# Kernel tuning notes

Hardware: AMD Instinct MI355X
Metric: run time of the kernel (lower is better)

## Reference

```python
import jax, jax.numpy as jnp
import numpy as np

B, S, D, P, W = 16, 100, 8192, 100, 3  # batch, seq, feat dim, proj width, window size


def setup_inputs() -> dict:
    key = jax.random.key(0)
    ks = jax.random.split(key, 6)
    return {
        "x": jax.random.normal(ks[0], (B, S, D), dtype=jnp.float32),
        "wq": jax.random.normal(ks[1], (D, P), dtype=jnp.float32) * (1.0 / np.sqrt(D)),
        "wk": jax.random.normal(ks[2], (D, P), dtype=jnp.float32) * (1.0 / np.sqrt(D)),
        "wv": jax.random.normal(ks[3], (D, P), dtype=jnp.float32) * (1.0 / np.sqrt(D)),
        "forwardpad": jax.random.normal(ks[4], (B, 1, D), dtype=jnp.float32),
        "backwardpad": jax.random.normal(ks[5], (B, 1, D), dtype=jnp.float32),
    }


def reference(x, wq, wk, wv, forwardpad, backwardpad):
    # pad: (B, S+2, D)
    padded = jnp.concatenate([forwardpad, x, backwardpad], axis=1)
    # gather all 100 overlapping size-3 windows at once: (B, S, W, D)
    idx = jnp.arange(S)[:, None] + jnp.arange(W)[None, :]  # (S, W)
    windows = padded[:, idx, :]
    # shared projections across all windows (original recomputed per window)
    q = jnp.einsum("bswd,dp->bswp", windows, wq)
    k = jnp.einsum("bswd,dp->bswp", windows, wk)
    v = jnp.einsum("bswd,dp->bswp", windows, wv)
    # per-window 3x3 attention
    scores = jnp.einsum("bswp,bsup->bswu", q, k)  # (B, S, W, W)
    attn = jax.nn.softmax(scores, axis=-1)
    out = jnp.einsum("bswu,bsup->bswp", attn, v)  # (B, S, W, P)
    # original concatenates windows along seq then takes [:, 1::3, :] -> center token of each window
    return out[:, :, 1, :]  # (B, S, P)
```

## Files before the change

kernel.cpp:

```cpp
#include <hip/hip_runtime.h>
#include <hip/hip_bf16.h>
#include <hip/hip_fp16.h>

constexpr int Dk   = 8192;
constexpr int Bb   = 16;
constexpr int Ss   = 100;
constexpr int Pp   = 100;
constexpr int MROW = 1632;
constexpr int NT   = 20;
constexpr int NCC  = 320;
constexpr int NQ   = 304;
constexpr int KG   = 1024;
constexpr int KC   = 16;
constexpr int CH   = 5;
constexpr int MBL  = 52;

constexpr size_t B_SEG   = (size_t)NT * KG * 128;
constexpr size_t PSTRIDE = (size_t)1664 * NCC;

typedef short s8v __attribute__((ext_vector_type(8)));
typedef short s4v __attribute__((ext_vector_type(4)));
typedef float f4v __attribute__((ext_vector_type(4)));

__device__ inline unsigned short f2bf_rne(float f) {
    unsigned u = __float_as_uint(f);
    u += 0x7fffu + ((u >> 16) & 1u);
    return (unsigned short)(u >> 16);
}

__global__ __launch_bounds__(256) void pack_b(
    const float* __restrict__ wq, const float* __restrict__ wk,
    const float* __restrict__ wv,
    short* __restrict__ b_hi, short* __restrict__ b_lo) {
    const int id = blockIdx.x * 256 + threadIdx.x;
    const int n  = id % NCC;
    const int kg = id / NCC;
    if (kg >= KG) return;

    const float* w = nullptr; int p = 0;
    if (n < 100)      { w = wq; p = n; }
    else if (n < 200) { w = wk; p = n - 100; }
    else if (n < 300) { w = wv; p = n - 200; }

    s8v hi, lo;
    #pragma unroll
    for (int j = 0; j < 8; ++j) {
        const float v = w ? w[(size_t)(kg * 8 + j) * Pp + p] : 0.0f;
        const unsigned u = __float_as_uint(v);
        hi[j] = (short)(unsigned short)(u >> 16);
        const float hf = __uint_as_float(u & 0xffff0000u);
        lo[j] = (short)f2bf_rne(v - hf);
    }
    const size_t doff = ((size_t)(n >> 4) * KG + kg) * 128 + (size_t)(n & 15) * 8;
    *(s8v*)(b_hi + doff) = hi;
    *(s8v*)(b_lo + doff) = lo;
}

__global__ __launch_bounds__(256, 2) void qkv_gemm(
    const float* __restrict__ x, const float* __restrict__ fpad,
    const float* __restrict__ bpad,
    const short* __restrict__ b_hi, const short* __restrict__ b_lo,
    unsigned short* __restrict__ part) {
    __shared__ __align__(16) short ahis[2][1024];
    __shared__ __align__(16) short alos[2][1024];

    const int id   = blockIdx.x;
    const int xcd  = id & 7;
    const int slot = id >> 3;
    const int half = (slot >= 52) ? 1 : 0;
    const int kc   = xcd * 2 + half;
    const int mb   = slot - half * 52;

    const int tid  = threadIdx.x;
    const int w    = tid >> 6;
    const int l    = tid & 63;
    const int m    = l & 15;
    const int quad = l >> 4;

    const int sr  = tid >> 3;
    const int skq = tid & 7;
    const float* sp;
    {
        const int r = mb * 32 + sr;
        if (r >= MROW) sp = fpad;
        else {
            const int b = r / 102, rr = r - b * 102;
            if (rr == 0)        sp = fpad + (size_t)b * Dk;
            else if (rr == 101) sp = bpad + (size_t)b * Dk;
            else                sp = x + ((size_t)b * Ss + (rr - 1)) * Dk;
        }
        sp += kc * 512 + skq * 4;
    }
    const int woff = ((sr >> 4) * 4 + (skq >> 1)) * 128 + (sr & 15) * 8 + (skq & 1) * 4;

    float4 av[4];
    #pragma unroll
    for (int p = 0; p < 4; ++p) av[p] = *(const float4*)(sp + p * 32);

    s8v bh[2][5], bl[2][5];
    {
        const int kg0 = kc * 64 + quad;
        #pragma unroll
        for (int j = 0; j < 5; ++j) {
            const size_t bo = ((size_t)(w * 5 + j) * KG + kg0) * 128 + (size_t)m * 8;
            bh[0][j] = *(const s8v*)(b_hi + bo);
            bl[0][j] = *(const s8v*)(b_lo + bo);
        }
    }

    f4v acc[2][5];
    #pragma unroll
    for (int i = 0; i < 2; ++i)
        #pragma unroll
        for (int j = 0; j < 5; ++j) {
            f4v z = {0.f, 0.f, 0.f, 0.f};
            acc[i][j] = z;
        }

    #pragma unroll
    for (int s = 0; s < 16; ++s) {
        const int cur = s & 1, nxt = cur ^ 1;

        const float4 va = av[s & 3];

        if (s < 15) {
            const int kgn = kc * 64 + (s + 1) * 4 + quad;
            #pragma unroll
            for (int j = 0; j < 5; ++j) {
                const size_t bo = ((size_t)(w * 5 + j) * KG + kgn) * 128 + (size_t)m * 8;
                bh[nxt][j] = *(const s8v*)(b_hi + bo);
                bl[nxt][j] = *(const s8v*)(b_lo + bo);
            }
        }
        if (s < 12) av[s & 3] = *(const float4*)(sp + (s + 4) * 32);

        __builtin_amdgcn_sched_barrier(0);

        const float vv[4] = {va.x, va.y, va.z, va.w};
        s4v h4, l4;
        #pragma unroll
        for (int jj = 0; jj < 4; ++jj) {
            const unsigned u = __float_as_uint(vv[jj]);
            h4[jj] = (short)(unsigned short)(u >> 16);
            l4[jj] = (short)f2bf_rne(vv[jj] - __uint_as_float(u & 0xffff0000u));
        }

        *(s4v*)&ahis[cur][woff] = h4;
        *(s4v*)&alos[cur][woff] = l4;

        asm volatile("s_waitcnt lgkmcnt(0)\n\ts_barrier" ::: "memory");

        const s8v ah0 = *(const s8v*)&ahis[cur][(quad * 16 + m) * 8];
        const s8v ah1 = *(const s8v*)&ahis[cur][((4 + quad) * 16 + m) * 8];
        const s8v al0 = *(const s8v*)&alos[cur][(quad * 16 + m) * 8];
        const s8v al1 = *(const s8v*)&alos[cur][((4 + quad) * 16 + m) * 8];

        #pragma unroll
        for (int j = 0; j < 5; ++j) {
            const s8v bhv = bh[cur][j], blv = bl[cur][j];
            acc[0][j] = __builtin_amdgcn_mfma_f32_16x16x32_bf16(ah0, bhv, acc[0][j], 0, 0, 0);
            acc[1][j] = __builtin_amdgcn_mfma_f32_16x16x32_bf16(ah1, bhv, acc[1][j], 0, 0, 0);
            acc[0][j] = __builtin_amdgcn_mfma_f32_16x16x32_bf16(al0, bhv, acc[0][j], 0, 0, 0);
            acc[1][j] = __builtin_amdgcn_mfma_f32_16x16x32_bf16(al1, bhv, acc[1][j], 0, 0, 0);
            acc[0][j] = __builtin_amdgcn_mfma_f32_16x16x32_bf16(ah0, blv, acc[0][j], 0, 0, 0);
            acc[1][j] = __builtin_amdgcn_mfma_f32_16x16x32_bf16(ah1, blv, acc[1][j], 0, 0, 0);
        }
    }

    unsigned short* __restrict__ pout = part + (size_t)kc * PSTRIDE;
    #pragma unroll
    for (int i = 0; i < 2; ++i) {
        #pragma unroll
        for (int j = 0; j < 5; ++j) {
            const int col  = (w * 5 + j) * 16 + m;
            const int row0 = mb * 32 + i * 16 + quad * 4;
            #pragma unroll
            for (int r = 0; r < 4; ++r)
                pout[(size_t)(row0 + r) * NCC + col] =
                    __half_as_ushort(__float2half(acc[i][j][r]));
        }
    }
}

__global__ __launch_bounds__(256) void reduce_k(
    const unsigned short* __restrict__ part, float* __restrict__ qkv) {
    const int t = blockIdx.x * 256 + threadIdx.x;
    const int row = t / 40;
    const int col0 = (t - row * 40) * 8;
    const size_t base = (size_t)row * NCC + col0;

    float sum[8] = {0.f, 0.f, 0.f, 0.f, 0.f, 0.f, 0.f, 0.f};
    #pragma unroll
    for (int k = 0; k < KC; ++k) {
        const s8v u = *(const s8v*)(part + (size_t)k * PSTRIDE + base);
        #pragma unroll
        for (int ii = 0; ii < 8; ++ii)
            sum[ii] += __half2float(__ushort_as_half((unsigned short)u[ii]));
    }
    if (col0 < NQ) {
        f4v a = {sum[0], sum[1], sum[2], sum[3]};
        f4v b = {sum[4], sum[5], sum[6], sum[7]};
        *(f4v*)(qkv + (size_t)row * NQ + col0)     = a;
        *(f4v*)(qkv + (size_t)row * NQ + col0 + 4) = b;
    }
}

__global__ __launch_bounds__(256) void attn3(
    const float* __restrict__ qkv, float* __restrict__ out) {
    const int blk = blockIdx.x;
    const int b  = blk / (Ss / CH);
    const int c  = blk % (Ss / CH);
    const int s0 = c * CH;
    const int tid = threadIdx.x;

    __shared__ float red[CH + 2][304];
    __shared__ float sc[CH][3];

    for (int idx = tid; idx < (CH + 2) * 300; idx += 256) {
        const int row = idx / 300, col = idx % 300;
        red[row][col] = qkv[(size_t)(b * 102 + s0 + row) * NQ + col];
    }
    __syncthreads();

    if (tid < CH * 3 * 16) {
        const int d = tid >> 4, g = tid & 15;
        const int ss = d / 3, u = d % 3;
        float ps = 0.0f;
        #pragma unroll
        for (int t = 0; t < 7; ++t) {
            const int p = g + t * 16;
            if (p < Pp) ps += red[ss + 1][p] * red[ss + u][100 + p];
        }
        #pragma unroll
        for (int off = 8; off > 0; off >>= 1) ps += __shfl_down(ps, off, 16);
        if (g == 0) sc[ss][u] = ps;
    }
    __syncthreads();

    for (int idx = tid; idx < CH * Pp; idx += 256) {
        const int ss = idx / Pp, p = idx % Pp;
        const float a0 = sc[ss][0], a1 = sc[ss][1], a2 = sc[ss][2];
        const float mx = fmaxf(a0, fmaxf(a1, a2));
        const float e0 = __expf(a0 - mx), e1 = __expf(a1 - mx), e2 = __expf(a2 - mx);
        const float inv = 1.0f / (e0 + e1 + e2);
        out[(size_t)(b * Ss + s0 + ss) * Pp + p] =
            inv * (e0 * red[ss][200 + p] + e1 * red[ss + 1][200 + p] +
                   e2 * red[ss + 2][200 + p]);
    }
}

extern "C" void kernel_launch(void* const* d_in, const int* in_sizes, int n_in,
                              void* d_out, int out_size, void* d_ws, size_t ws_size,
                              hipStream_t stream) {
    const float* x    = (const float*)d_in[0];
    const float* wq   = (const float*)d_in[1];
    const float* wk   = (const float*)d_in[2];
    const float* wv   = (const float*)d_in[3];
    const float* fpad = (const float*)d_in[4];
    const float* bpad = (const float*)d_in[5];
    float* out = (float*)d_out;

    short* b_hi = (short*)d_ws;
    short* b_lo = b_hi + B_SEG;
    unsigned short* part = (unsigned short*)(b_lo + B_SEG);
    float* qkv = (float*)(part + (size_t)KC * PSTRIDE);

    pack_b<<<(NCC * KG) / 256, 256, 0, stream>>>(wq, wk, wv, b_hi, b_lo);
    qkv_gemm<<<MBL * KC, 256, 0, stream>>>(x, fpad, bpad, b_hi, b_lo, part);
    reduce_k<<<260, 256, 0, stream>>>(part, qkv);
    attn3<<<Bb * (Ss / CH), 256, 0, stream>>>(qkv, out);
}
```

Baseline: 143.1 us.

## Double GEMM M-tile to 64 rows per block to halve B-fragment reloads

Each qkv_gemm block now covers 64 rows of the padded activation matrix instead of 32, so each block issues twice as many MFMAs per B fragment loaded from global memory. Grid size drops from 832 to 416 blocks, and each thread converts 8 floats per step with wider LDS stores. This reduces total B-matrix traffic and the number of barriers per FLOP. In exchange it needs 40 more accumulator registers and twice the LDS, which may lower occupancy, and the smaller grid may leave compute units underfilled. The sched_barrier that separated loads from compute is also removed.

```diff
diff --git a/kernel.cpp b/kernel.cpp
--- a/kernel.cpp
+++ b/kernel.cpp
@@ -13,7 +13,7 @@
 constexpr int KG   = 1024;
 constexpr int KC   = 16;
 constexpr int CH   = 5;
-constexpr int MBL  = 52;
+constexpr int MBL2 = 26;
 
 constexpr size_t B_SEG   = (size_t)NT * KG * 128;
 constexpr size_t PSTRIDE = (size_t)1664 * NCC;
@@ -61,15 +61,15 @@
     const float* __restrict__ bpad,
     const short* __restrict__ b_hi, const short* __restrict__ b_lo,
     unsigned short* __restrict__ part) {
-    __shared__ __align__(16) short ahis[2][1024];
-    __shared__ __align__(16) short alos[2][1024];
+    __shared__ __align__(16) short ahis[2][2048];
+    __shared__ __align__(16) short alos[2][2048];
 
     const int id   = blockIdx.x;
     const int xcd  = id & 7;
     const int slot = id >> 3;
-    const int half = (slot >= 52) ? 1 : 0;
+    const int half = (slot >= MBL2) ? 1 : 0;
     const int kc   = xcd * 2 + half;
-    const int mb   = slot - half * 52;
+    const int mb   = slot - half * MBL2;
 
     const int tid  = threadIdx.x;
     const int w    = tid >> 6;
@@ -77,11 +77,11 @@
     const int m    = l & 15;
     const int quad = l >> 4;
 
-    const int sr  = tid >> 3;
-    const int skq = tid & 7;
+    const int sr  = tid >> 2;
+    const int skq = tid & 3;
     const float* sp;
     {
-        const int r = mb * 32 + sr;
+        const int r = mb * 64 + sr;
         if (r >= MROW) sp = fpad;
         else {
             const int b = r / 102, rr = r - b * 102;
@@ -89,13 +89,16 @@
             else if (rr == 101) sp = bpad + (size_t)b * Dk;
             else                sp = x + ((size_t)b * Ss + (rr - 1)) * Dk;
         }
-        sp += kc * 512 + skq * 4;
-    }
-    const int woff = ((sr >> 4) * 4 + (skq >> 1)) * 128 + (sr & 15) * 8 + (skq & 1) * 4;
-
-    float4 av[4];
-    #pragma unroll
-    for (int p = 0; p < 4; ++p) av[p] = *(const float4*)(sp + p * 32);
+        sp += kc * 512 + skq * 8;
+    }
+    const int woff = ((sr >> 4) * 4 + skq) * 128 + (sr & 15) * 8;
+
+    float4 av0[2], av1[2];
+    #pragma unroll
+    for (int p = 0; p < 2; ++p) {
+        av0[p] = *(const float4*)(sp + p * 32);
+        av1[p] = *(const float4*)(sp + p * 32 + 4);
+    }
 
     s8v bh[2][5], bl[2][5];
     {
@@ -108,9 +111,9 @@
         }
     }
 
-    f4v acc[2][5];
-    #pragma unroll
-    for (int i = 0; i < 2; ++i)
+    f4v acc[4][5];
+    #pragma unroll
+    for (int i = 0; i < 4; ++i)
         #pragma unroll
         for (int j = 0; j < 5; ++j) {
             f4v z = {0.f, 0.f, 0.f, 0.f};
@@ -121,7 +124,8 @@
     for (int s = 0; s < 16; ++s) {
         const int cur = s & 1, nxt = cur ^ 1;
 
-        const float4 va = av[s & 3];
+        const float4 va0 = av0[s & 1];
+        const float4 va1 = av1[s & 1];
 
         if (s < 15) {
             const int kgn = kc * 64 + (s + 1) * 4 + quad;
@@ -132,48 +136,55 @@
                 bl[nxt][j] = *(const s8v*)(b_lo + bo);
             }
         }
-        if (s < 12) av[s & 3] = *(const float4*)(sp + (s + 4) * 32);
-
-        __builtin_amdgcn_sched_barrier(0);
-
-        const float vv[4] = {va.x, va.y, va.z, va.w};
-        s4v h4, l4;
-        #pragma unroll
-        for (int jj = 0; jj < 4; ++jj) {
+        if (s < 14) {
+            av0[s & 1] = *(const float4*)(sp + (s + 2) * 32);
+            av1[s & 1] = *(const float4*)(sp + (s + 2) * 32 + 4);
+        }
+
+        const float vv[8] = {va0.x, va0.y, va0.z, va0.w,
+                             va1.x, va1.y, va1.z, va1.w};
+        s8v h8, l8;
+        #pragma unroll
+        for (int jj = 0; jj < 8; ++jj) {
             const unsigned u = __float_as_uint(vv[jj]);
-            h4[jj] = (short)(unsigned short)(u >> 16);
-            l4[jj] = (short)f2bf_rne(vv[jj] - __uint_as_float(u & 0xffff0000u));
-        }
-
-        *(s4v*)&ahis[cur][woff] = h4;
-        *(s4v*)&alos[cur][woff] = l4;
+            h8[jj] = (short)(unsigned short)(u >> 16);
+            l8[jj] = (short)f2bf_rne(vv[jj] - __uint_as_float(u & 0xffff0000u));
+        }
+
+        *(s8v*)&ahis[cur][woff] = h8;
+        *(s8v*)&alos[cur][woff] = l8;
 
         asm volatile("s_waitcnt lgkmcnt(0)\n\ts_barrier" ::: "memory");
 
-        const s8v ah0 = *(const s8v*)&ahis[cur][(quad * 16 + m) * 8];
-        const s8v ah1 = *(const s8v*)&ahis[cur][((4 + quad) * 16 + m) * 8];
-        const s8v al0 = *(const s8v*)&alos[cur][(quad * 16 + m) * 8];
-        const s8v al1 = *(const s8v*)&alos[cur][((4 + quad) * 16 + m) * 8];
+        s8v ah[4], al[4];
+        #pragma unroll
+        for (int i = 0; i < 4; ++i) {
+            ah[i] = *(const s8v*)&ahis[cur][((i * 4 + quad) * 16 + m) * 8];
+            al[i] = *(const s8v*)&alos[cur][((i * 4 + quad) * 16 + m) * 8];
+        }
 
         #pragma unroll
         for (int j = 0; j < 5; ++j) {
             const s8v bhv = bh[cur][j], blv = bl[cur][j];
-            acc[0][j] = __builtin_amdgcn_mfma_f32_16x16x32_bf16(ah0, bhv, acc[0][j], 0, 0, 0);
-            acc[1][j] = __builtin_amdgcn_mfma_f32_16x16x32_bf16(ah1, bhv, acc[1][j], 0, 0, 0);
-            acc[0][j] = __builtin_amdgcn_mfma_f32_16x16x32_bf16(al0, bhv, acc[0][j], 0, 0, 0);
-            acc[1][j] = __builtin_amdgcn_mfma_f32_16x16x32_bf16(al1, bhv, acc[1][j], 0, 0, 0);
-            acc[0][j] = __builtin_amdgcn_mfma_f32_16x16x32_bf16(ah0, blv, acc[0][j], 0, 0, 0);
-            acc[1][j] = __builtin_amdgcn_mfma_f32_16x16x32_bf16(ah1, blv, acc[1][j], 0, 0, 0);
+            #pragma unroll
+            for (int i = 0; i < 4; ++i)
+                acc[i][j] = __builtin_amdgcn_mfma_f32_16x16x32_bf16(ah[i], bhv, acc[i][j], 0, 0, 0);
+            #pragma unroll
+            for (int i = 0; i < 4; ++i)
+                acc[i][j] = __builtin_amdgcn_mfma_f32_16x16x32_bf16(al[i], bhv, acc[i][j], 0, 0, 0);
+            #pragma unroll
+            for (int i = 0; i < 4; ++i)
+                acc[i][j] = __builtin_amdgcn_mfma_f32_16x16x32_bf16(ah[i], blv, acc[i][j], 0, 0, 0);
         }
     }
 
     unsigned short* __restrict__ pout = part + (size_t)kc * PSTRIDE;
     #pragma unroll
-    for (int i = 0; i < 2; ++i) {
+    for (int i = 0; i < 4; ++i) {
         #pragma unroll
         for (int j = 0; j < 5; ++j) {
             const int col  = (w * 5 + j) * 16 + m;
-            const int row0 = mb * 32 + i * 16 + quad * 4;
+            const int row0 = mb * 64 + i * 16 + quad * 4;
             #pragma unroll
             for (int r = 0; r < 4; ++r)
                 pout[(size_t)(row0 + r) * NCC + col] =
@@ -266,7 +277,7 @@
     float* qkv = (float*)(part + (size_t)KC * PSTRIDE);
 
     pack_b<<<(NCC * KG) / 256, 256, 0, stream>>>(wq, wk, wv, b_hi, b_lo);
-    qkv_gemm<<<MBL * KC, 256, 0, stream>>>(x, fpad, bpad, b_hi, b_lo, part);
+    qkv_gemm<<<MBL2 * KC, 256, 0, stream>>>(x, fpad, bpad, b_hi, b_lo, part);
     reduce_k<<<260, 256, 0, stream>>>(part, qkv);
     attn3<<<Bb * (Ss / CH), 256, 0, stream>>>(qkv, out);
 }
```

After: 134.8 us. 5.8% less time.
